# Performance work log

Measured on AMD Instinct MI355X. Metric: run time of the kernel, lower is better.

Reference implementation:

```python
import jax, jax.numpy as jnp
import numpy as np

NGQ = 5
_XK, _WK = np.polynomial.hermite.hermgauss(NGQ)  # Gauss-Hermite nodes/weights
N = 4_194_304   # observations
Q = 100_000     # number of random-effect groups (categories)


def setup_inputs() -> dict:
    key = jax.random.key(0)
    k1, k2, k3 = jax.random.split(key, 3)
    # binary outcomes (logistic GLMM)
    y_true = jax.random.randint(k1, (N, 1), 0, 2).astype(jnp.float32)
    # fixed-effect predictor (logits) from the network
    y_pred = jax.random.normal(k2, (N, 1), dtype=jnp.float32)
    # group id per observation
    Z_idx = jax.random.randint(k3, (N,), 0, Q).astype(jnp.int64)
    # learned random-intercept variance (the layer's sig2bs variable)
    sig2b = jnp.ones((1,), dtype=jnp.float32)
    return {"y_true": y_true, "y_pred": y_pred, "Z_idx": Z_idx, "sig2b": sig2b}


def reference(y_true, y_pred, Z_idx, sig2b):
    # Faithful vectorized form of NLL.custom_loss_glm:
    #   loss = -sum_i log( sum_k w_k/sqrt(pi) * exp(y_i^T f_i + sum(y_i)*c_k
    #                                              - sum(log(1+exp(f_i + c_k)))) )
    # where c_k = sqrt(2)*sqrt(sig2b)*x_k and i runs over groups.
    # Empty groups contribute log(sum_k w_k/sqrt(pi)) = log(1) = 0, so using
    # num_segments=Q matches the original loop over unique ids exactly.
    y = y_true[:, 0]
    f = y_pred[:, 0]
    seg = Z_idx
    dt = f.dtype
    xk = jnp.asarray(_XK, dt)                      # [K]
    wk = jnp.asarray(_WK, dt)                      # [K]
    ck = jnp.sqrt(jnp.asarray(2.0, dt)) * jnp.sqrt(sig2b[0]) * xk  # [K]

    yf = jax.ops.segment_sum(y * f, seg, num_segments=Q)   # [Q]  y_i^T f_i
    sy = jax.ops.segment_sum(y, seg, num_segments=Q)       # [Q]  sum(y_i)
    # log(1+exp(f + c_k)) per quadrature node, summed per group -> [K, Q]
    sp = jax.nn.softplus(f[None, :] + ck[:, None])          # [K, N]
    lg = jax.vmap(lambda s: jax.ops.segment_sum(s, seg, num_segments=Q))(sp)

    inv_sqrt_pi = jnp.asarray(1.0 / np.sqrt(np.pi), dt)
    k_sum = jnp.sum(
        jnp.exp(yf[None, :] + sy[None, :] * ck[:, None] - lg)
        * (wk[:, None] * inv_sqrt_pi),
        axis=0,
    )                                                       # [Q]
    return -jnp.sum(jnp.log(k_sum))
```

## Files before the change

### kernel.cpp

```cpp
#include <hip/hip_runtime.h>
#include <hip/hip_fp16.h>
#include <math.h>

#define Q_SEG 100000
#define NGQ   5
#define NBIN  500
#define SPB   200
#define CAP   12288
#define LCAP  9216
#define SCT   1024

__device__ __forceinline__ void gh5(float* xk, float* wk) {
    xk[0] = -2.0201828704560856f; xk[1] = -0.9585724646138185f; xk[2] = 0.0f;
    xk[3] =  0.9585724646138185f; xk[4] =  2.0201828704560856f;
    wk[0] = 0.019953242059045913f; wk[1] = 0.3936193231522412f; wk[2] = 0.9453087204829419f;
    wk[3] = 0.3936193231522412f;   wk[4] = 0.019953242059045913f;
}

__device__ __forceinline__ float fast_softplus(float x) {
    return fmaxf(x, 0.0f) + __logf(1.0f + __expf(-fabsf(x)));
}

__global__ void k_init(unsigned* __restrict__ cursors) {
    int j = blockIdx.x * blockDim.x + threadIdx.x;
    if (j < NBIN) cursors[j] = (unsigned)(j * CAP);
}

__global__ __launch_bounds__(SCT)
void k_scatter(const float* __restrict__ y_true, const float* __restrict__ y_pred,
               const int* __restrict__ Z, unsigned* __restrict__ cursors,
               unsigned* __restrict__ rec, int n) {
    __shared__ unsigned lh[NBIN];
    __shared__ unsigned lc[NBIN];
    const int per = (n + gridDim.x - 1) / gridDim.x;
    const int lo  = blockIdx.x * per;
    int hi = lo + per; if (hi > n) hi = n;

    for (int j = threadIdx.x; j < NBIN; j += SCT) lh[j] = 0;
    __syncthreads();
    for (int i = lo + threadIdx.x; i < hi; i += SCT) {
        int q = Z[i];
        if ((unsigned)q < (unsigned)Q_SEG) atomicAdd(&lh[q / SPB], 1u);
    }
    __syncthreads();
    for (int j = threadIdx.x; j < NBIN; j += SCT)
        lc[j] = lh[j] ? atomicAdd(&cursors[j], lh[j]) : 0u;
    __syncthreads();
    for (int i = lo + threadIdx.x; i < hi; i += SCT) {
        int q = Z[i];
        if ((unsigned)q < (unsigned)Q_SEG) {
            int bin = q / SPB;
            unsigned lq = (unsigned)(q - bin * SPB);
            float y = y_true[i];
            float f = y_pred[i];
            unsigned pos = atomicAdd(&lc[bin], 1u);
            if (pos < (unsigned)((bin + 1) * CAP)) {
                unsigned hb = (unsigned)__half_as_ushort(__float2half(f));
                rec[pos] = (hb << 16) | (lq << 1) | (y != 0.0f ? 1u : 0u);
            }
        }
    }
}

__global__ __launch_bounds__(SCT)
void k_main(const unsigned* __restrict__ rec, const unsigned* __restrict__ cursors,
            const float* __restrict__ sig2b, float* __restrict__ out) {
    __shared__ unsigned srt[LCAP];
    __shared__ unsigned hist[SPB];
    __shared__ unsigned sc[256];
    __shared__ unsigned pstart[SPB];
    __shared__ unsigned cur[SPB];
    __shared__ float    acc[SPB * 7];
    __shared__ float    red[16];

    const int t = threadIdx.x;
    const int b = blockIdx.x;

    for (int j = t; j < SPB; j += SCT) hist[j] = 0;
    for (int j = t; j < SPB * 7; j += SCT) acc[j] = 0.0f;
    __syncthreads();

    const unsigned gstart = (unsigned)(b * CAP);
    unsigned gend = cursors[b];
    const unsigned cap_end = gstart + CAP;
    if (gend > cap_end) gend = cap_end;

    for (unsigned i = gstart + t; i < gend; i += SCT)
        atomicAdd(&hist[(rec[i] >> 1) & 0x1FFu], 1u);
    __syncthreads();

    if (t < 256) sc[t] = (t < SPB) ? hist[t] : 0u;
    __syncthreads();
    #pragma unroll
    for (int off = 1; off < 256; off <<= 1) {
        unsigned add = 0;
        if (t < 256 && t >= off) add = sc[t - off];
        __syncthreads();
        if (t < 256) sc[t] += add;
        __syncthreads();
    }
    if (t < SPB) {
        unsigned ps = sc[t] - hist[t];
        pstart[t] = ps;
        cur[t] = ps;
    }
    __syncthreads();

    float xk[NGQ], wk[NGQ];
    gh5(xk, wk);
    const float scale = sqrtf(2.0f * sig2b[0]);

    for (unsigned i = gstart + t; i < gend; i += SCT) {
        unsigned r  = rec[i];
        unsigned lq = (r >> 1) & 0x1FFu;
        unsigned p  = atomicAdd(&cur[lq], 1u);
        if (p < (unsigned)LCAP) {
            srt[p] = r;
        } else {
            float f = __half2float(__ushort_as_half((unsigned short)(r >> 16)));
            float* seg = &acc[lq * 7];
            if (r & 1u) { atomicAdd(&seg[0], f); atomicAdd(&seg[1], 1.0f); }
            #pragma unroll
            for (int k = 0; k < NGQ; ++k)
                atomicAdd(&seg[2 + k], fast_softplus(fmaf(scale, xk[k], f)));
        }
    }
    __syncthreads();

    float contrib = 0.0f;
    if (t < SPB) {
        float s0 = 0.0f, s1 = 0.0f, l0 = 0.0f, l1 = 0.0f, l2 = 0.0f, l3 = 0.0f, l4 = 0.0f;
        unsigned jb = pstart[t];
        unsigned je = cur[t];
        if (jb > (unsigned)LCAP) jb = LCAP;
        if (je > (unsigned)LCAP) je = LCAP;
        for (unsigned j = jb; j < je; ++j) {
            unsigned r = srt[j];
            float f = __half2float(__ushort_as_half((unsigned short)(r >> 16)));
            if (r & 1u) { s0 += f; s1 += 1.0f; }
            l0 += fast_softplus(fmaf(scale, xk[0], f));
            l1 += fast_softplus(fmaf(scale, xk[1], f));
            l2 += fast_softplus(fmaf(scale, xk[2], f));
            l3 += fast_softplus(fmaf(scale, xk[3], f));
            l4 += fast_softplus(fmaf(scale, xk[4], f));
        }
        const float* v = &acc[t * 7];
        s0 += v[0]; s1 += v[1];
        l0 += v[2]; l1 += v[3]; l2 += v[4]; l3 += v[5]; l4 += v[6];

        const float inv_sqrt_pi = 0.5641895835477563f;
        float a[NGQ] = {
            s0 + s1 * (scale * xk[0]) - l0,
            s0 + s1 * (scale * xk[1]) - l1,
            s0 + s1 * (scale * xk[2]) - l2,
            s0 + s1 * (scale * xk[3]) - l3,
            s0 + s1 * (scale * xk[4]) - l4
        };
        float m = a[0];
        #pragma unroll
        for (int k = 1; k < NGQ; ++k) m = fmaxf(m, a[k]);
        float ks = 0.0f;
        #pragma unroll
        for (int k = 0; k < NGQ; ++k) ks += wk[k] * expf(a[k] - m);
        contrib = -(m + logf(ks * inv_sqrt_pi));
    }

    #pragma unroll
    for (int off = 32; off > 0; off >>= 1)
        contrib += __shfl_down(contrib, off, 64);
    int lane = t & 63, wid = t >> 6;
    if (lane == 0) red[wid] = contrib;
    __syncthreads();
    if (t == 0) {
        float s = 0.0f;
        #pragma unroll
        for (int w = 0; w < 16; ++w) s += red[w];
        atomicAdd(out, s);
    }
}

__global__ void nll_pass1(const float* __restrict__ y_true,
                          const float* __restrict__ y_pred,
                          const int*   __restrict__ Z_idx,
                          const float* __restrict__ sig2b,
                          float* __restrict__ yf, float* __restrict__ sy,
                          float* __restrict__ lg, int n) {
    float xk[NGQ], wk[NGQ];
    gh5(xk, wk);
    const float s = sqrtf(2.0f * sig2b[0]);
    int i = blockIdx.x * blockDim.x + threadIdx.x;
    if (i >= n) return;
    float y = y_true[i];
    float f = y_pred[i];
    int   q = Z_idx[i];
    if ((unsigned)q >= (unsigned)Q_SEG) return;
    if (y != 0.0f) {
        atomicAdd(&yf[q], y * f);
        atomicAdd(&sy[q], y);
    }
    #pragma unroll
    for (int k = 0; k < NGQ; ++k) {
        float x  = f + s * xk[k];
        float sp = fmaxf(x, 0.0f) + log1pf(expf(-fabsf(x)));
        atomicAdd(&lg[k * Q_SEG + q], sp);
    }
}

__global__ void nll_pass2(const float* __restrict__ yf,
                          const float* __restrict__ sy,
                          const float* __restrict__ lg,
                          const float* __restrict__ sig2b,
                          float* __restrict__ out) {
    float xk[NGQ], wk[NGQ];
    gh5(xk, wk);
    const float s = sqrtf(2.0f * sig2b[0]);
    const float inv_sqrt_pi = 0.5641895835477563f;
    int q = blockIdx.x * blockDim.x + threadIdx.x;
    float contrib = 0.0f;
    if (q < Q_SEG) {
        float yfv = yf[q], syv = sy[q];
        float a[NGQ];
        float m = -1e30f;
        #pragma unroll
        for (int k = 0; k < NGQ; ++k) {
            a[k] = yfv + syv * (s * xk[k]) - lg[k * Q_SEG + q];
            m = fmaxf(m, a[k]);
        }
        float ks = 0.0f;
        #pragma unroll
        for (int k = 0; k < NGQ; ++k) ks += wk[k] * expf(a[k] - m);
        contrib = -(m + logf(ks * inv_sqrt_pi));
    }
    #pragma unroll
    for (int off = 32; off > 0; off >>= 1)
        contrib += __shfl_down(contrib, off, 64);
    __shared__ float red[4];
    int lane = threadIdx.x & 63;
    int wid  = threadIdx.x >> 6;
    if (lane == 0) red[wid] = contrib;
    __syncthreads();
    if (threadIdx.x == 0) {
        float t = 0.0f;
        int nw = (blockDim.x + 63) >> 6;
        for (int w = 0; w < nw; ++w) t += red[w];
        atomicAdd(out, t);
    }
}

extern "C" void kernel_launch(void* const* d_in, const int* in_sizes, int n_in,
                              void* d_out, int out_size, void* d_ws, size_t ws_size,
                              hipStream_t stream) {
    const float* y_true = (const float*)d_in[0];
    const float* y_pred = (const float*)d_in[1];
    const int*   Z_idx  = (const int*)d_in[2];
    const float* sig2b  = (const float*)d_in[3];
    float* out = (float*)d_out;
    int n = in_sizes[0];

    hipMemsetAsync(d_out, 0, sizeof(float), stream);

    const size_t recBytes = (size_t)NBIN * CAP * sizeof(unsigned);
    const size_t need = recBytes + 1024 * sizeof(unsigned);
    if (ws_size >= need) {
        unsigned* rec     = (unsigned*)d_ws;
        unsigned* cursors = (unsigned*)((char*)d_ws + recBytes);
        k_init<<<2, 256, 0, stream>>>(cursors);
        k_scatter<<<256, SCT, 0, stream>>>(y_true, y_pred, Z_idx, cursors, rec, n);
        k_main<<<NBIN, SCT, 0, stream>>>(rec, cursors, sig2b, out);
    } else {
        float* yf = (float*)d_ws;
        float* sy = yf + Q_SEG;
        float* lg = sy + Q_SEG;
        hipMemsetAsync(d_ws, 0, (size_t)(2 + NGQ) * Q_SEG * sizeof(float), stream);
        int threads = 256;
        nll_pass1<<<(n + threads - 1) / threads, threads, 0, stream>>>(
            y_true, y_pred, Z_idx, sig2b, yf, sy, lg, n);
        nll_pass2<<<(Q_SEG + threads - 1) / threads, threads, 0, stream>>>(
            yf, sy, lg, sig2b, out);
    }
}
```

Baseline: 161.5 us.

## Stage scatter records in LDS by bin for coalesced global writes, vectorize loads

The scatter kernel now processes fixed 8192-element chunks per block (512 blocks instead of 256), sorts packed records locally in shared memory by bin via a wavefront-shuffle prefix scan, and then writes them contiguously to the global bin buffers. This replaces random per-element global writes with mostly contiguous runs. Both kernels switch to int4/float4 vectorized loads, and the main kernel's multi-barrier shared-memory scan is replaced by a single-wavefront shuffle scan. The cost is more shared memory per scatter block and an extra LDS pass.

After: 141.2 us. 1.14x faster.

```diff
diff --git a/kernel.cpp b/kernel.cpp
--- a/kernel.cpp
+++ b/kernel.cpp
@@ -9,6 +9,7 @@
 #define CAP   12288
 #define LCAP  9216
 #define SCT   1024
+#define SEPB  8192
 
 __device__ __forceinline__ void gh5(float* xk, float* wk) {
     xk[0] = -2.0201828704560856f; xk[1] = -0.9585724646138185f; xk[2] = 0.0f;
@@ -21,6 +22,11 @@
     return fmaxf(x, 0.0f) + __logf(1.0f + __expf(-fabsf(x)));
 }
 
+__device__ __forceinline__ unsigned pack_rec(float f, float y, unsigned lq) {
+    unsigned hb = (unsigned)__half_as_ushort(__float2half(f));
+    return (hb << 16) | (lq << 1) | (y != 0.0f ? 1u : 0u);
+}
+
 __global__ void k_init(unsigned* __restrict__ cursors) {
     int j = blockIdx.x * blockDim.x + threadIdx.x;
     if (j < NBIN) cursors[j] = (unsigned)(j * CAP);
@@ -30,35 +36,94 @@
 void k_scatter(const float* __restrict__ y_true, const float* __restrict__ y_pred,
                const int* __restrict__ Z, unsigned* __restrict__ cursors,
                unsigned* __restrict__ rec, int n) {
+    __shared__ unsigned       srt[SEPB];
+    __shared__ unsigned short sbin[SEPB];
     __shared__ unsigned lh[NBIN];
-    __shared__ unsigned lc[NBIN];
-    const int per = (n + gridDim.x - 1) / gridDim.x;
-    const int lo  = blockIdx.x * per;
-    int hi = lo + per; if (hi > n) hi = n;
-
-    for (int j = threadIdx.x; j < NBIN; j += SCT) lh[j] = 0;
-    __syncthreads();
-    for (int i = lo + threadIdx.x; i < hi; i += SCT) {
-        int q = Z[i];
+    __shared__ unsigned lstart[NBIN];
+    __shared__ unsigned lcur[NBIN];
+    __shared__ unsigned gbase[NBIN];
+
+    const int t  = threadIdx.x;
+    const int lo = blockIdx.x * SEPB;
+    int hi = lo + SEPB; if (hi > n) hi = n;
+    const int cnt  = hi - lo;
+    const int cnt4 = cnt & ~3;
+
+    for (int j = t; j < NBIN; j += SCT) lh[j] = 0;
+    __syncthreads();
+
+    for (int p = t * 4; p < cnt4; p += SCT * 4) {
+        int4 z4 = *(const int4*)(Z + lo + p);
+        int qs[4] = {z4.x, z4.y, z4.z, z4.w};
+        #pragma unroll
+        for (int j = 0; j < 4; ++j)
+            if ((unsigned)qs[j] < (unsigned)Q_SEG) atomicAdd(&lh[qs[j] / SPB], 1u);
+    }
+    for (int p = cnt4 + t; p < cnt; p += SCT) {
+        int q = Z[lo + p];
         if ((unsigned)q < (unsigned)Q_SEG) atomicAdd(&lh[q / SPB], 1u);
     }
     __syncthreads();
-    for (int j = threadIdx.x; j < NBIN; j += SCT)
-        lc[j] = lh[j] ? atomicAdd(&cursors[j], lh[j]) : 0u;
-    __syncthreads();
-    for (int i = lo + threadIdx.x; i < hi; i += SCT) {
-        int q = Z[i];
+
+    if (t < 64) {
+        unsigned run = 0;
+        #pragma unroll
+        for (int c = 0; c < (NBIN + 63) / 64; ++c) {
+            int idx = c * 64 + t;
+            unsigned h = (idx < NBIN) ? lh[idx] : 0u;
+            unsigned v = h;
+            #pragma unroll
+            for (int off = 1; off < 64; off <<= 1) {
+                unsigned u = __shfl_up(v, off, 64);
+                if (t >= off) v += u;
+            }
+            if (idx < NBIN) { unsigned ex = run + v - h; lstart[idx] = ex; lcur[idx] = ex; }
+            run += __shfl(v, 63, 64);
+        }
+    }
+    __syncthreads();
+
+    for (int j = t; j < NBIN; j += SCT)
+        gbase[j] = lh[j] ? atomicAdd(&cursors[j], lh[j]) : 0u;
+    __syncthreads();
+
+    for (int p = t * 4; p < cnt4; p += SCT * 4) {
+        int4   z4 = *(const int4*)(Z + lo + p);
+        float4 y4 = *(const float4*)(y_true + lo + p);
+        float4 f4 = *(const float4*)(y_pred + lo + p);
+        int   qs[4] = {z4.x, z4.y, z4.z, z4.w};
+        float ys[4] = {y4.x, y4.y, y4.z, y4.w};
+        float fs[4] = {f4.x, f4.y, f4.z, f4.w};
+        #pragma unroll
+        for (int j = 0; j < 4; ++j) {
+            int q = qs[j];
+            if ((unsigned)q < (unsigned)Q_SEG) {
+                int bin = q / SPB;
+                unsigned lq = (unsigned)(q - bin * SPB);
+                unsigned slot = atomicAdd(&lcur[bin], 1u);
+                srt[slot]  = pack_rec(fs[j], ys[j], lq);
+                sbin[slot] = (unsigned short)bin;
+            }
+        }
+    }
+    for (int p = cnt4 + t; p < cnt; p += SCT) {
+        int q = Z[lo + p];
         if ((unsigned)q < (unsigned)Q_SEG) {
             int bin = q / SPB;
             unsigned lq = (unsigned)(q - bin * SPB);
-            float y = y_true[i];
-            float f = y_pred[i];
-            unsigned pos = atomicAdd(&lc[bin], 1u);
-            if (pos < (unsigned)((bin + 1) * CAP)) {
-                unsigned hb = (unsigned)__half_as_ushort(__float2half(f));
-                rec[pos] = (hb << 16) | (lq << 1) | (y != 0.0f ? 1u : 0u);
-            }
-        }
+            unsigned slot = atomicAdd(&lcur[bin], 1u);
+            srt[slot]  = pack_rec(y_pred[lo + p], y_true[lo + p], lq);
+            sbin[slot] = (unsigned short)bin;
+        }
+    }
+    __syncthreads();
+
+    const int total = lcur[NBIN - 1];
+    for (int j = t; j < total; j += SCT) {
+        unsigned r = srt[j];
+        unsigned b = (unsigned)sbin[j];
+        unsigned dst = gbase[b] + (unsigned)(j - lstart[b]);
+        if (dst < (b + 1u) * CAP) rec[dst] = r;
     }
 }
 
@@ -67,7 +132,6 @@
             const float* __restrict__ sig2b, float* __restrict__ out) {
     __shared__ unsigned srt[LCAP];
     __shared__ unsigned hist[SPB];
-    __shared__ unsigned sc[256];
     __shared__ unsigned pstart[SPB];
     __shared__ unsigned cur[SPB];
     __shared__ float    acc[SPB * 7];
@@ -84,25 +148,34 @@
     unsigned gend = cursors[b];
     const unsigned cap_end = gstart + CAP;
     if (gend > cap_end) gend = cap_end;
-
-    for (unsigned i = gstart + t; i < gend; i += SCT)
-        atomicAdd(&hist[(rec[i] >> 1) & 0x1FFu], 1u);
-    __syncthreads();
-
-    if (t < 256) sc[t] = (t < SPB) ? hist[t] : 0u;
-    __syncthreads();
-    #pragma unroll
-    for (int off = 1; off < 256; off <<= 1) {
-        unsigned add = 0;
-        if (t < 256 && t >= off) add = sc[t - off];
-        __syncthreads();
-        if (t < 256) sc[t] += add;
-        __syncthreads();
-    }
-    if (t < SPB) {
-        unsigned ps = sc[t] - hist[t];
-        pstart[t] = ps;
-        cur[t] = ps;
+    const unsigned cnt  = gend - gstart;
+    const unsigned cnt4 = cnt & ~3u;
+
+    for (unsigned p = t * 4; p < cnt4; p += SCT * 4) {
+        int4 r4 = *(const int4*)(rec + gstart + p);
+        unsigned rs[4] = {(unsigned)r4.x, (unsigned)r4.y, (unsigned)r4.z, (unsigned)r4.w};
+        #pragma unroll
+        for (int j = 0; j < 4; ++j) atomicAdd(&hist[(rs[j] >> 1) & 0x1FFu], 1u);
+    }
+    for (unsigned p = cnt4 + t; p < cnt; p += SCT)
+        atomicAdd(&hist[(rec[gstart + p] >> 1) & 0x1FFu], 1u);
+    __syncthreads();
+
+    if (t < 64) {
+        unsigned run = 0;
+        #pragma unroll
+        for (int c = 0; c < (SPB + 63) / 64; ++c) {
+            int idx = c * 64 + t;
+            unsigned h = (idx < SPB) ? hist[idx] : 0u;
+            unsigned v = h;
+            #pragma unroll
+            for (int off = 1; off < 64; off <<= 1) {
+                unsigned u = __shfl_up(v, off, 64);
+                if (t >= off) v += u;
+            }
+            if (idx < SPB) { unsigned ex = run + v - h; pstart[idx] = ex; cur[idx] = ex; }
+            run += __shfl(v, 63, 64);
+        }
     }
     __syncthreads();
 
@@ -110,12 +183,32 @@
     gh5(xk, wk);
     const float scale = sqrtf(2.0f * sig2b[0]);
 
-    for (unsigned i = gstart + t; i < gend; i += SCT) {
-        unsigned r  = rec[i];
+    for (unsigned p = t * 4; p < cnt4; p += SCT * 4) {
+        int4 r4 = *(const int4*)(rec + gstart + p);
+        unsigned rs[4] = {(unsigned)r4.x, (unsigned)r4.y, (unsigned)r4.z, (unsigned)r4.w};
+        #pragma unroll
+        for (int j = 0; j < 4; ++j) {
+            unsigned r  = rs[j];
+            unsigned lq = (r >> 1) & 0x1FFu;
+            unsigned pp = atomicAdd(&cur[lq], 1u);
+            if (pp < (unsigned)LCAP) {
+                srt[pp] = r;
+            } else {
+                float f = __half2float(__ushort_as_half((unsigned short)(r >> 16)));
+                float* seg = &acc[lq * 7];
+                if (r & 1u) { atomicAdd(&seg[0], f); atomicAdd(&seg[1], 1.0f); }
+                #pragma unroll
+                for (int k = 0; k < NGQ; ++k)
+                    atomicAdd(&seg[2 + k], fast_softplus(fmaf(scale, xk[k], f)));
+            }
+        }
+    }
+    for (unsigned p = cnt4 + t; p < cnt; p += SCT) {
+        unsigned r  = rec[gstart + p];
         unsigned lq = (r >> 1) & 0x1FFu;
-        unsigned p  = atomicAdd(&cur[lq], 1u);
-        if (p < (unsigned)LCAP) {
-            srt[p] = r;
+        unsigned pp = atomicAdd(&cur[lq], 1u);
+        if (pp < (unsigned)LCAP) {
+            srt[pp] = r;
         } else {
             float f = __half2float(__ushort_as_half((unsigned short)(r >> 16)));
             float* seg = &acc[lq * 7];
@@ -265,7 +358,8 @@
         unsigned* rec     = (unsigned*)d_ws;
         unsigned* cursors = (unsigned*)((char*)d_ws + recBytes);
         k_init<<<2, 256, 0, stream>>>(cursors);
-        k_scatter<<<256, SCT, 0, stream>>>(y_true, y_pred, Z_idx, cursors, rec, n);
+        int sgrid = (n + SEPB - 1) / SEPB;
+        k_scatter<<<sgrid, SCT, 0, stream>>>(y_true, y_pred, Z_idx, cursors, rec, n);
         k_main<<<NBIN, SCT, 0, stream>>>(rec, cursors, sig2b, out);
     } else {
         float* yf = (float*)d_ws;
```
